# Optimization experiments

Measured on AMD Instinct MI355X. Metric: run time of the kernel, lower is better.

The kernel has to match this reference:

```python
import jax, jax.numpy as jnp
import numpy as np

H = 64  # hidden_size


def gru_layer(x, h0, W_ih, W_hh, b_ih, b_hh):
    """PyTorch-convention GRU layer. x: [B,T,D], h0: [B,H]. Returns ([B,T,H], [B,H])."""
    # Precompute input-side gate projections with one big GEMM: [B,T,3H]
    gx_all = jnp.einsum('btd,gd->btg', x, W_ih) + b_ih

    def step(h, gx):
        gh = h @ W_hh.T + b_hh                      # [B,3H]
        xr, xz, xn = jnp.split(gx, 3, axis=-1)
        hr, hz, hn = jnp.split(gh, 3, axis=-1)
        r = jax.nn.sigmoid(xr + hr)
        z = jax.nn.sigmoid(xz + hz)
        n = jnp.tanh(xn + r * hn)
        h_new = (1.0 - z) * n + z * h
        return h_new, h_new

    hT, hs = jax.lax.scan(step, h0, jnp.swapaxes(gx_all, 0, 1))  # hs: [T,B,H]
    return jnp.swapaxes(hs, 0, 1), hT


def setup_inputs() -> dict:
    key = jax.random.key(0)
    ks = jax.random.split(key, 16)
    B, T, D = 256, 2048, 1
    x = jax.random.normal(ks[0], (B, T, D), dtype=jnp.float32)
    h0 = jnp.zeros((2, B, H), dtype=jnp.float32)
    s = 1.0 / np.sqrt(H)
    # Layer 0: input_size=1
    W_ih0 = jax.random.normal(ks[1], (3 * H, D), dtype=jnp.float32) * s
    W_hh0 = jax.random.normal(ks[2], (3 * H, H), dtype=jnp.float32) * s
    b_ih0 = jnp.zeros((3 * H,), dtype=jnp.float32)
    b_hh0 = jnp.zeros((3 * H,), dtype=jnp.float32)
    # Layer 1: input_size=H
    W_ih1 = jax.random.normal(ks[3], (3 * H, H), dtype=jnp.float32) * s
    W_hh1 = jax.random.normal(ks[4], (3 * H, H), dtype=jnp.float32) * s
    b_ih1 = jnp.zeros((3 * H,), dtype=jnp.float32)
    b_hh1 = jnp.zeros((3 * H,), dtype=jnp.float32)
    # Head: Linear(H,H) -> ReLU -> Linear(H,1)
    Wh1 = jax.random.normal(ks[5], (H, H), dtype=jnp.float32) * s
    bh1 = jnp.zeros((H,), dtype=jnp.float32)
    Wh2 = jax.random.normal(ks[6], (1, H), dtype=jnp.float32) * s
    bh2 = jnp.zeros((1,), dtype=jnp.float32)
    return {"x": x, "h0": h0, "W_ih0": W_ih0, "W_hh0": W_hh0, "b_ih0": b_ih0,
            "b_hh0": b_hh0, "W_ih1": W_ih1, "W_hh1": W_hh1, "b_ih1": b_ih1,
            "b_hh1": b_hh1, "Wh1": Wh1, "bh1": bh1, "Wh2": Wh2, "bh2": bh2}


def reference(x, h0, W_ih0, W_hh0, b_ih0, b_hh0, W_ih1, W_hh1, b_ih1, b_hh1,
              Wh1, bh1, Wh2, bh2):
    z0, hT0 = gru_layer(x, h0[0], W_ih0, W_hh0, b_ih0, b_hh0)
    z1, hT1 = gru_layer(z0, h0[1], W_ih1, W_hh1, b_ih1, b_hh1)
    hT = jnp.stack([hT0, hT1], axis=0)           # [2,B,H]
    h = jax.nn.relu(jnp.einsum('bth,oh->bto', z1, Wh1) + bh1)
    y = jnp.einsum('bth,oh->bto', h, Wh2) + bh2  # [B,T,1]
    return (y, hT)
```

## Files before the change

kernel.cpp:

```cpp
#include <hip/hip_runtime.h>

#define HH 64
#define G3 192
#define TT 2048
#define BB 256
#define YSZ (BB*TT)

__device__ __forceinline__ float sigmoid_f(float v) {
    return 1.0f / (1.0f + __expf(-v));
}
__device__ __forceinline__ float tanh_f(float v) {
    return 1.0f - 2.0f / (1.0f + __expf(2.0f * v));
}

__global__ __launch_bounds__(256, 1)
void gru_fused(const float* __restrict__ x,
               const float* __restrict__ h0in,
               const float* __restrict__ W_ih0,
               const float* __restrict__ W_hh0,
               const float* __restrict__ b_ih0,
               const float* __restrict__ b_hh0,
               const float* __restrict__ W_ih1,
               const float* __restrict__ W_hh1,
               const float* __restrict__ b_ih1,
               const float* __restrict__ b_hh1,
               const float* __restrict__ Wh1,
               const float* __restrict__ bh1,
               const float* __restrict__ Wh2,
               const float* __restrict__ bh2,
               float* __restrict__ out)
{
    const int b   = blockIdx.x;
    const int tid = threadIdx.x;

    __shared__ __align__(16) float h0_lds[HH];
    __shared__ __align__(16) float h1_lds[HH];
    __shared__ __align__(16) float gh0_lds[G3];
    __shared__ __align__(16) float gx1_lds[G3];
    __shared__ __align__(16) float gh1_lds[G3];
    __shared__ __align__(16) float x_lds[TT];

    {
        const float4* xs = reinterpret_cast<const float4*>(x + (size_t)b * TT);
        float4*       xd = reinterpret_cast<float4*>(x_lds);
        for (int k = tid; k < TT/4; k += 256) xd[k] = xs[k];
    }
    if (tid < HH) {
        h0_lds[tid] = h0in[          b*HH + tid];
        h1_lds[tid] = h0in[BB*HH +   b*HH + tid];
    }

    float w0[HH], wi1[HH], wh1r[HH];
    float bias_gh0 = 0.f, bias_gx1 = 0.f, bias_gh1 = 0.f;
    float wh2_r = 0.f, bias_head = 0.f, bh2_s = 0.f;
    float wih0_r=0.f, wih0_z=0.f, wih0_n=0.f, bih0_r=0.f, bih0_z=0.f, bih0_n=0.f;

    if (tid < G3) {
        #pragma unroll
        for (int k = 0; k < 16; ++k) {
            float4 v;
            v = reinterpret_cast<const float4*>(W_hh0 + tid*HH)[k];
            w0  [4*k]=v.x; w0  [4*k+1]=v.y; w0  [4*k+2]=v.z; w0  [4*k+3]=v.w;
            v = reinterpret_cast<const float4*>(W_ih1 + tid*HH)[k];
            wi1 [4*k]=v.x; wi1 [4*k+1]=v.y; wi1 [4*k+2]=v.z; wi1 [4*k+3]=v.w;
            v = reinterpret_cast<const float4*>(W_hh1 + tid*HH)[k];
            wh1r[4*k]=v.x; wh1r[4*k+1]=v.y; wh1r[4*k+2]=v.z; wh1r[4*k+3]=v.w;
        }
        bias_gh0 = b_hh0[tid];
        bias_gx1 = b_ih1[tid];
        bias_gh1 = b_hh1[tid];
    } else {
        const int j = tid - G3;
        #pragma unroll
        for (int k = 0; k < 16; ++k) {
            float4 v = reinterpret_cast<const float4*>(Wh1 + j*HH)[k];
            w0[4*k]=v.x; w0[4*k+1]=v.y; w0[4*k+2]=v.z; w0[4*k+3]=v.w;
        }
        wh2_r     = Wh2[j];
        bias_head = bh1[j];
        bh2_s     = bh2[0];
    }
    if (tid >= 64 && tid < 128) {
        const int j = tid - 64;
        wih0_r = W_ih0[j];        bih0_r = b_ih0[j];
        wih0_z = W_ih0[j+64];     bih0_z = b_ih0[j+64];
        wih0_n = W_ih0[j+128];    bih0_n = b_ih0[j+128];
    }

    __syncthreads();

    const float4* h04 = reinterpret_cast<const float4*>(h0_lds);
    const float4* h14 = reinterpret_cast<const float4*>(h1_lds);

    for (int i = 0; i <= TT + 1; ++i) {
        if (tid < G3) {
            float a0 = bias_gh0, a1 = bias_gx1, a2 = bias_gh1;
            #pragma unroll
            for (int k = 0; k < 16; ++k) {
                float4 u = h04[k];
                float4 v = h14[k];
                a0 = fmaf(w0  [4*k+0], u.x, a0);
                a1 = fmaf(wi1 [4*k+0], u.x, a1);
                a2 = fmaf(wh1r[4*k+0], v.x, a2);
                a0 = fmaf(w0  [4*k+1], u.y, a0);
                a1 = fmaf(wi1 [4*k+1], u.y, a1);
                a2 = fmaf(wh1r[4*k+1], v.y, a2);
                a0 = fmaf(w0  [4*k+2], u.z, a0);
                a1 = fmaf(wi1 [4*k+2], u.z, a1);
                a2 = fmaf(wh1r[4*k+2], v.z, a2);
                a0 = fmaf(w0  [4*k+3], u.w, a0);
                a1 = fmaf(wi1 [4*k+3], u.w, a1);
                a2 = fmaf(wh1r[4*k+3], v.w, a2);
            }
            gh0_lds[tid] = a0;
            gx1_lds[tid] = a1;
            gh1_lds[tid] = a2;
        } else {
            float s = bias_head;
            #pragma unroll
            for (int k = 0; k < 16; ++k) {
                float4 v = h14[k];
                s = fmaf(w0[4*k+0], v.x, s);
                s = fmaf(w0[4*k+1], v.y, s);
                s = fmaf(w0[4*k+2], v.z, s);
                s = fmaf(w0[4*k+3], v.w, s);
            }
            float p = fmaxf(s, 0.f) * wh2_r;
            #pragma unroll
            for (int m = 1; m < 64; m <<= 1) p += __shfl_xor(p, m, 64);
            if (tid == G3 && i >= 2) {
                out[(size_t)b * TT + (i - 2)] = p + bh2_s;
            }
        }
        __syncthreads();

        if (tid < 64) {
            const int j = tid;
            float xr = gx1_lds[j], xz = gx1_lds[j+64], xn = gx1_lds[j+128];
            float hr = gh1_lds[j], hz = gh1_lds[j+64], hn = gh1_lds[j+128];
            float r = sigmoid_f(xr + hr);
            float z = sigmoid_f(xz + hz);
            float n = tanh_f(fmaf(r, hn, xn));
            float hprev = h1_lds[j];
            float hnew  = fmaf(z, hprev - n, n);
            if (i >= 1 && i <= TT) h1_lds[j] = hnew;
        } else if (tid < 128) {
            const int j  = tid - 64;
            const int xi = (i < TT) ? i : (TT - 1);
            float xv = x_lds[xi];
            float xr = fmaf(xv, wih0_r, bih0_r);
            float xz = fmaf(xv, wih0_z, bih0_z);
            float xn = fmaf(xv, wih0_n, bih0_n);
            float hr = gh0_lds[j], hz = gh0_lds[j+64], hn = gh0_lds[j+128];
            float r = sigmoid_f(xr + hr);
            float z = sigmoid_f(xz + hz);
            float n = tanh_f(fmaf(r, hn, xn));
            float hprev = h0_lds[j];
            float hnew  = fmaf(z, hprev - n, n);
            if (i < TT) h0_lds[j] = hnew;
        }
        __syncthreads();
    }

    if (tid < HH) {
        out[YSZ +            b*HH + tid] = h0_lds[tid];
        out[YSZ + BB*HH +    b*HH + tid] = h1_lds[tid];
    }
}

extern "C" void kernel_launch(void* const* d_in, const int* in_sizes, int n_in,
                              void* d_out, int out_size, void* d_ws, size_t ws_size,
                              hipStream_t stream) {
    const float* x     = (const float*)d_in[0];
    const float* h0in  = (const float*)d_in[1];
    const float* W_ih0 = (const float*)d_in[2];
    const float* W_hh0 = (const float*)d_in[3];
    const float* b_ih0 = (const float*)d_in[4];
    const float* b_hh0 = (const float*)d_in[5];
    const float* W_ih1 = (const float*)d_in[6];
    const float* W_hh1 = (const float*)d_in[7];
    const float* b_ih1 = (const float*)d_in[8];
    const float* b_hh1 = (const float*)d_in[9];
    const float* Wh1   = (const float*)d_in[10];
    const float* bh1   = (const float*)d_in[11];
    const float* Wh2   = (const float*)d_in[12];
    const float* bh2   = (const float*)d_in[13];
    float* out = (float*)d_out;

    gru_fused<<<dim3(BB), dim3(256), 0, stream>>>(
        x, h0in, W_ih0, W_hh0, b_ih0, b_hh0,
        W_ih1, W_hh1, b_ih1, b_hh1, Wh1, bh1, Wh2, bh2, out);
}
```

Baseline: 1.819 ms.

## Split GRU recurrent dot products across two thread halves with LDS partial sums

Doubles the block to 512 threads and splits each 64-wide recurrent dot product into two 32-wide halves, each half writing partial sums to shared memory, which the gate threads then add. The head's ReLU/reduction moves to a separate wavefront after the barrier. The aim is to halve the serial FMA chain per step on the latency-bound recurrence and cut register pressure per thread. In exchange it adds more shared-memory traffic, a larger barrier across 8 wavefronts, and an extra reduction read per gate.

```diff
diff --git a/kernel.cpp b/kernel.cpp
--- a/kernel.cpp
+++ b/kernel.cpp
@@ -1,7 +1,6 @@
 #include <hip/hip_runtime.h>
 
 #define HH 64
-#define G3 192
 #define TT 2048
 #define BB 256
 #define YSZ (BB*TT)
@@ -13,7 +12,7 @@
     return 1.0f - 2.0f / (1.0f + __expf(2.0f * v));
 }
 
-__global__ __launch_bounds__(256, 1)
+__global__ __launch_bounds__(512, 2)
 void gru_fused(const float* __restrict__ x,
                const float* __restrict__ h0in,
                const float* __restrict__ W_ih0,
@@ -30,141 +29,127 @@
                const float* __restrict__ bh2,
                float* __restrict__ out)
 {
-    const int b   = blockIdx.x;
-    const int tid = threadIdx.x;
+    const int b    = blockIdx.x;
+    const int tid  = threadIdx.x;
+    const int t    = tid & 255;
+    const int half = tid >> 8;
+    const int ko   = half << 5;
 
     __shared__ __align__(16) float h0_lds[HH];
     __shared__ __align__(16) float h1_lds[HH];
-    __shared__ __align__(16) float gh0_lds[G3];
-    __shared__ __align__(16) float gx1_lds[G3];
-    __shared__ __align__(16) float gh1_lds[G3];
+    __shared__ __align__(16) float part[2 * 192 * 4];
+    __shared__ __align__(16) float ph[2 * 64];
     __shared__ __align__(16) float x_lds[TT];
 
     {
         const float4* xs = reinterpret_cast<const float4*>(x + (size_t)b * TT);
         float4*       xd = reinterpret_cast<float4*>(x_lds);
-        for (int k = tid; k < TT/4; k += 256) xd[k] = xs[k];
+        for (int k = tid; k < TT / 4; k += 512) xd[k] = xs[k];
     }
     if (tid < HH) {
-        h0_lds[tid] = h0in[          b*HH + tid];
-        h1_lds[tid] = h0in[BB*HH +   b*HH + tid];
+        h0_lds[tid] = h0in[           b * HH + tid];
+        h1_lds[tid] = h0in[BB * HH +  b * HH + tid];
     }
 
-    float w0[HH], wi1[HH], wh1r[HH];
-    float bias_gh0 = 0.f, bias_gx1 = 0.f, bias_gh1 = 0.f;
-    float wh2_r = 0.f, bias_head = 0.f, bh2_s = 0.f;
-    float wih0_r=0.f, wih0_z=0.f, wih0_n=0.f, bih0_r=0.f, bih0_z=0.f, bih0_n=0.f;
-
-    if (tid < G3) {
+    float4 wA[8], wB[8], wC[8];
+    float bA = 0.f, bB = 0.f, bC = 0.f;
+    if (t < 192) {
+        const float4* pa = reinterpret_cast<const float4*>(W_hh0 + t * HH + ko);
+        const float4* pb = reinterpret_cast<const float4*>(W_ih1 + t * HH + ko);
+        const float4* pc = reinterpret_cast<const float4*>(W_hh1 + t * HH + ko);
         #pragma unroll
-        for (int k = 0; k < 16; ++k) {
-            float4 v;
-            v = reinterpret_cast<const float4*>(W_hh0 + tid*HH)[k];
-            w0  [4*k]=v.x; w0  [4*k+1]=v.y; w0  [4*k+2]=v.z; w0  [4*k+3]=v.w;
-            v = reinterpret_cast<const float4*>(W_ih1 + tid*HH)[k];
-            wi1 [4*k]=v.x; wi1 [4*k+1]=v.y; wi1 [4*k+2]=v.z; wi1 [4*k+3]=v.w;
-            v = reinterpret_cast<const float4*>(W_hh1 + tid*HH)[k];
-            wh1r[4*k]=v.x; wh1r[4*k+1]=v.y; wh1r[4*k+2]=v.z; wh1r[4*k+3]=v.w;
-        }
-        bias_gh0 = b_hh0[tid];
-        bias_gx1 = b_ih1[tid];
-        bias_gh1 = b_hh1[tid];
+        for (int k = 0; k < 8; ++k) { wA[k] = pa[k]; wB[k] = pb[k]; wC[k] = pc[k]; }
+        if (half == 0) { bA = b_hh0[t]; bB = b_ih1[t]; bC = b_hh1[t]; }
     } else {
-        const int j = tid - G3;
+        const float4* pa = reinterpret_cast<const float4*>(Wh1 + (t - 192) * HH + ko);
         #pragma unroll
-        for (int k = 0; k < 16; ++k) {
-            float4 v = reinterpret_cast<const float4*>(Wh1 + j*HH)[k];
-            w0[4*k]=v.x; w0[4*k+1]=v.y; w0[4*k+2]=v.z; w0[4*k+3]=v.w;
-        }
-        wh2_r     = Wh2[j];
-        bias_head = bh1[j];
-        bh2_s     = bh2[0];
+        for (int k = 0; k < 8; ++k) { wA[k] = pa[k]; wB[k] = pa[k]; wC[k] = pa[k]; }
     }
+    float wih0_r = 0.f, wih0_z = 0.f, wih0_n = 0.f;
+    float bih0_r = 0.f, bih0_z = 0.f, bih0_n = 0.f;
     if (tid >= 64 && tid < 128) {
         const int j = tid - 64;
-        wih0_r = W_ih0[j];        bih0_r = b_ih0[j];
-        wih0_z = W_ih0[j+64];     bih0_z = b_ih0[j+64];
-        wih0_n = W_ih0[j+128];    bih0_n = b_ih0[j+128];
+        wih0_r = W_ih0[j];       bih0_r = b_ih0[j];
+        wih0_z = W_ih0[j + 64];  bih0_z = b_ih0[j + 64];
+        wih0_n = W_ih0[j + 128]; bih0_n = b_ih0[j + 128];
+    }
+    float wh2_r = 0.f, bhead = 0.f, bh2_s = 0.f;
+    if (tid >= 448) {
+        const int j = tid - 448;
+        wh2_r = Wh2[j]; bhead = bh1[j]; bh2_s = bh2[0];
     }
 
     __syncthreads();
 
-    const float4* h04 = reinterpret_cast<const float4*>(h0_lds);
-    const float4* h14 = reinterpret_cast<const float4*>(h1_lds);
+    const float4* h0q   = reinterpret_cast<const float4*>(h0_lds + ko);
+    const float4* h1q   = reinterpret_cast<const float4*>(h1_lds + ko);
+    float4*       part4 = reinterpret_cast<float4*>(part);
 
     for (int i = 0; i <= TT + 1; ++i) {
-        if (tid < G3) {
-            float a0 = bias_gh0, a1 = bias_gx1, a2 = bias_gh1;
+        if (t < 192) {
+            float a0 = bA, a1 = bB, a2 = bC;
             #pragma unroll
-            for (int k = 0; k < 16; ++k) {
-                float4 u = h04[k];
-                float4 v = h14[k];
-                a0 = fmaf(w0  [4*k+0], u.x, a0);
-                a1 = fmaf(wi1 [4*k+0], u.x, a1);
-                a2 = fmaf(wh1r[4*k+0], v.x, a2);
-                a0 = fmaf(w0  [4*k+1], u.y, a0);
-                a1 = fmaf(wi1 [4*k+1], u.y, a1);
-                a2 = fmaf(wh1r[4*k+1], v.y, a2);
-                a0 = fmaf(w0  [4*k+2], u.z, a0);
-                a1 = fmaf(wi1 [4*k+2], u.z, a1);
-                a2 = fmaf(wh1r[4*k+2], v.z, a2);
-                a0 = fmaf(w0  [4*k+3], u.w, a0);
-                a1 = fmaf(wi1 [4*k+3], u.w, a1);
-                a2 = fmaf(wh1r[4*k+3], v.w, a2);
+            for (int k = 0; k < 8; ++k) {
+                float4 u = h0q[k];
+                float4 v = h1q[k];
+                a0 = fmaf(wA[k].x, u.x, a0); a1 = fmaf(wB[k].x, u.x, a1); a2 = fmaf(wC[k].x, v.x, a2);
+                a0 = fmaf(wA[k].y, u.y, a0); a1 = fmaf(wB[k].y, u.y, a1); a2 = fmaf(wC[k].y, v.y, a2);
+                a0 = fmaf(wA[k].z, u.z, a0); a1 = fmaf(wB[k].z, u.z, a1); a2 = fmaf(wC[k].z, v.z, a2);
+                a0 = fmaf(wA[k].w, u.w, a0); a1 = fmaf(wB[k].w, u.w, a1); a2 = fmaf(wC[k].w, v.w, a2);
             }
-            gh0_lds[tid] = a0;
-            gx1_lds[tid] = a1;
-            gh1_lds[tid] = a2;
+            part4[half * 192 + t] = make_float4(a0, a1, a2, 0.f);
         } else {
-            float s = bias_head;
+            float s = 0.f;
             #pragma unroll
-            for (int k = 0; k < 16; ++k) {
-                float4 v = h14[k];
-                s = fmaf(w0[4*k+0], v.x, s);
-                s = fmaf(w0[4*k+1], v.y, s);
-                s = fmaf(w0[4*k+2], v.z, s);
-                s = fmaf(w0[4*k+3], v.w, s);
+            for (int k = 0; k < 8; ++k) {
+                float4 v = h1q[k];
+                s = fmaf(wA[k].x, v.x, s); s = fmaf(wA[k].y, v.y, s);
+                s = fmaf(wA[k].z, v.z, s); s = fmaf(wA[k].w, v.w, s);
             }
-            float p = fmaxf(s, 0.f) * wh2_r;
-            #pragma unroll
-            for (int m = 1; m < 64; m <<= 1) p += __shfl_xor(p, m, 64);
-            if (tid == G3 && i >= 2) {
-                out[(size_t)b * TT + (i - 2)] = p + bh2_s;
-            }
+            ph[half * 64 + (t - 192)] = s;
         }
         __syncthreads();
 
         if (tid < 64) {
             const int j = tid;
-            float xr = gx1_lds[j], xz = gx1_lds[j+64], xn = gx1_lds[j+128];
-            float hr = gh1_lds[j], hz = gh1_lds[j+64], hn = gh1_lds[j+128];
-            float r = sigmoid_f(xr + hr);
-            float z = sigmoid_f(xz + hz);
-            float n = tanh_f(fmaf(r, hn, xn));
-            float hprev = h1_lds[j];
-            float hnew  = fmaf(z, hprev - n, n);
-            if (i >= 1 && i <= TT) h1_lds[j] = hnew;
+            float4 q0r = part4[j];       float4 q1r = part4[192 + j];
+            float4 q0z = part4[j + 64];  float4 q1z = part4[192 + j + 64];
+            float4 q0n = part4[j + 128]; float4 q1n = part4[192 + j + 128];
+            float r = sigmoid_f(q0r.y + q1r.y + q0r.z + q1r.z);
+            float z = sigmoid_f(q0z.y + q1z.y + q0z.z + q1z.z);
+            float n = tanh_f(fmaf(r, q0n.z + q1n.z, q0n.y + q1n.y));
+            if (i >= 1 && i <= TT) {
+                float hp = h1_lds[j];
+                h1_lds[j] = fmaf(z, hp - n, n);
+            }
         } else if (tid < 128) {
             const int j  = tid - 64;
             const int xi = (i < TT) ? i : (TT - 1);
+            float4 q0r = part4[j];       float4 q1r = part4[192 + j];
+            float4 q0z = part4[j + 64];  float4 q1z = part4[192 + j + 64];
+            float4 q0n = part4[j + 128]; float4 q1n = part4[192 + j + 128];
             float xv = x_lds[xi];
-            float xr = fmaf(xv, wih0_r, bih0_r);
-            float xz = fmaf(xv, wih0_z, bih0_z);
-            float xn = fmaf(xv, wih0_n, bih0_n);
-            float hr = gh0_lds[j], hz = gh0_lds[j+64], hn = gh0_lds[j+128];
-            float r = sigmoid_f(xr + hr);
-            float z = sigmoid_f(xz + hz);
-            float n = tanh_f(fmaf(r, hn, xn));
-            float hprev = h0_lds[j];
-            float hnew  = fmaf(z, hprev - n, n);
-            if (i < TT) h0_lds[j] = hnew;
+            float r = sigmoid_f(fmaf(xv, wih0_r, bih0_r) + q0r.x + q1r.x);
+            float z = sigmoid_f(fmaf(xv, wih0_z, bih0_z) + q0z.x + q1z.x);
+            float n = tanh_f(fmaf(r, q0n.x + q1n.x, fmaf(xv, wih0_n, bih0_n)));
+            if (i < TT) {
+                float hp = h0_lds[j];
+                h0_lds[j] = fmaf(z, hp - n, n);
+            }
+        } else if (tid >= 448) {
+            const int j = tid - 448;
+            float s = ph[j] + ph[64 + j] + bhead;
+            float p = fmaxf(s, 0.f) * wh2_r;
+            #pragma unroll
+            for (int m = 1; m < 64; m <<= 1) p += __shfl_xor(p, m, 64);
+            if (tid == 448 && i >= 2) out[(size_t)b * TT + (i - 2)] = p + bh2_s;
         }
         __syncthreads();
     }
 
     if (tid < HH) {
-        out[YSZ +            b*HH + tid] = h0_lds[tid];
-        out[YSZ + BB*HH +    b*HH + tid] = h1_lds[tid];
+        out[YSZ +           b * HH + tid] = h0_lds[tid];
+        out[YSZ + BB * HH + b * HH + tid] = h1_lds[tid];
     }
 }
 
@@ -187,7 +172,7 @@
     const float* bh2   = (const float*)d_in[13];
     float* out = (float*)d_out;
 
-    gru_fused<<<dim3(BB), dim3(256), 0, stream>>>(
+    gru_fused<<<dim3(BB), dim3(512), 0, stream>>>(
         x, h0in, W_ih0, W_hh0, b_ih0, b_hh0,
         W_ih1, W_hh1, b_ih1, b_hh1, Wh1, bh1, Wh2, bh2, out);
 }
```

New measurement: 1.702 ms. 6.4% less time.
